# Kernel tuning notes

Measured on AMD Instinct MI355X. Metric: run time of the kernel, lower is better.

Reference implementation:

```python
import jax, jax.numpy as jnp
import numpy as np

N_NODES = 100_000
N_EDGES = 1_600_000
D_IN = 128
D_HID = 64   # hard-coded hidden width in Embedder.__init__
D_OUT = 128  # embed_dim
N_GRAPHS = 512


def setup_inputs() -> dict:
    key = jax.random.key(0)
    ks = jax.random.split(key, 10)
    x = jax.random.normal(ks[0], (N_NODES, D_IN), dtype=jnp.float32)
    edge_index = jax.random.randint(ks[1], (2, N_EDGES), 0, N_NODES, dtype=jnp.int64)
    batch_index = jnp.sort(jax.random.randint(ks[2], (N_NODES,), 0, N_GRAPHS, dtype=jnp.int64))
    def glorot(k, fan_in, fan_out):
        s = 1.0 / np.sqrt(fan_in)
        return jax.random.uniform(k, (fan_in, fan_out), jnp.float32, -s, s)
    # layer 1: SAGEConv(D_IN -> D_HID); layer 2: SAGEConv(D_HID -> D_OUT)
    return {
        "x": x,
        "W1_l": glorot(ks[3], D_IN, D_HID),   # applied to mean-aggregated neighbors
        "W1_r": glorot(ks[4], D_IN, D_HID),   # applied to root node
        "b1": jnp.zeros((D_HID,), jnp.float32),
        "W2_l": glorot(ks[5], D_HID, D_OUT),
        "W2_r": glorot(ks[6], D_HID, D_OUT),
        "b2": jnp.zeros((D_OUT,), jnp.float32),
        "edge_index": edge_index,
        "batch_index": batch_index,
    }


def _sage_conv(x, edge_index, W_l, W_r, b):
    # PyG SAGEConv with mean aggregation:
    # out_i = (mean_{j in N(i)} x_j) @ W_l + x_i @ W_r + b
    src, dst = edge_index[0], edge_index[1]
    n = x.shape[0]
    agg = jax.ops.segment_sum(x[src], dst, num_segments=n)          # [N, F]
    deg = jax.ops.segment_sum(jnp.ones((src.shape[0],), x.dtype), dst, num_segments=n)
    mean_nbr = agg / jnp.maximum(deg, 1.0)[:, None]
    return mean_nbr @ W_l + x @ W_r + b


def reference(x, W1_l, W1_r, b1, W2_l, W2_r, b2, edge_index, batch_index):
    h = _sage_conv(x, edge_index, W1_l, W1_r, b1)
    h = jax.nn.relu(h)
    h = _sage_conv(h, edge_index, W2_l, W2_r, b2)
    # F.dropout(p=0.5, training=False) -> identity in eval mode
    # gap: global mean pool per graph
    sums = jax.ops.segment_sum(h, batch_index, num_segments=N_GRAPHS)
    cnts = jax.ops.segment_sum(jnp.ones((h.shape[0],), h.dtype), batch_index, num_segments=N_GRAPHS)
    return sums / jnp.maximum(cnts, 1.0)[:, None]
```

## Files before the change

### kernel.cpp

```cpp
#include <hip/hip_runtime.h>

#define NN   100000
#define NE   1600000
#define DIN  128
#define DH   64
#define DOUT 128
#define NG   512

#define NB    391
#define PARTB 250
#define EPB   6400
#define CAP   5120

typedef short short8 __attribute__((ext_vector_type(8)));
typedef float floatx4 __attribute__((ext_vector_type(4)));

__device__ __forceinline__ unsigned short f2bf(float f) {
  unsigned b = __float_as_uint(f);
  b += 0x7FFF + ((b >> 16) & 1);
  return (unsigned short)(b >> 16);
}
__device__ __forceinline__ float bflo(unsigned u) {
  return __uint_as_float(u << 16);
}
__device__ __forceinline__ float bfhi(unsigned u) {
  return __uint_as_float(u & 0xFFFF0000u);
}
__device__ __forceinline__ unsigned pack2(float a, float b) {
  return (unsigned)f2bf(a) | ((unsigned)f2bf(b) << 16);
}

__global__ __launch_bounds__(256) void prep_kernel(
    int* __restrict__ gcur,
    const float* __restrict__ W1l, const float* __restrict__ W1r,
    short* __restrict__ wfrag, const int* __restrict__ batch,
    int* __restrict__ gs) {
  int b = blockIdx.x;
  if (b == 0) {
    for (int i = threadIdx.x; i < NB; i += 256) gcur[i] = i * CAP;
  } else if (b == 1) {
    for (int i = threadIdx.x; i < DIN * DH; i += 256) {
      int k = i >> 6, n = i & 63;
      int kt = k >> 5, kin = k & 31;
      int lane = ((kin >> 3) << 4) | (n & 15);
      int j8 = kin & 7;
      int jt = n >> 4;
      float wl = W1l[i], wr = W1r[i];
      unsigned bl_ = __float_as_uint(wl);
      unsigned br_ = __float_as_uint(wr);
      short hl = (short)(bl_ >> 16);
      short hr = (short)(br_ >> 16);
      float rl = wl - __uint_as_float(bl_ & 0xFFFF0000u);
      float rr = wr - __uint_as_float(br_ & 0xFFFF0000u);
      short ll = (short)(__float_as_uint(rl) >> 16);
      short lr = (short)(__float_as_uint(rr) >> 16);
      int base0 = (((kt * 2 + 0) * 4 + jt) * 2) * 512 + lane * 8 + j8;
      int base1 = (((kt * 2 + 1) * 4 + jt) * 2) * 512 + lane * 8 + j8;
      wfrag[base0]       = hl;
      wfrag[base0 + 512] = ll;
      wfrag[base1]       = hr;
      wfrag[base1 + 512] = lr;
    }
  } else {
    for (int g = threadIdx.x; g <= NG; g += 256) {
      if (g == NG) { gs[NG] = NN; continue; }
      int lo = 0, hi = NN;
      while (lo < hi) {
        int mid = (lo + hi) >> 1;
        if (batch[mid] < g) lo = mid + 1; else hi = mid;
      }
      gs[g] = lo;
    }
  }
}

__global__ __launch_bounds__(256, 4) void proj_part_kernel(
    const int* __restrict__ src, const int* __restrict__ dst,
    int* __restrict__ gcur, int* __restrict__ part,
    const float* __restrict__ x, const short* __restrict__ wfrag,
    const float* __restrict__ b1, unsigned short* __restrict__ xlb,
    unsigned short* __restrict__ xrb) {
  __shared__ short sB[16384];
  if (blockIdx.x < PARTB) {
    int* hist  = (int*)sB;
    int* base_ = hist + NB;
    int* lcur  = hist + 2 * NB;
    for (int i = threadIdx.x; i < NB; i += 256) hist[i] = 0;
    __syncthreads();
    int start = blockIdx.x * EPB;
    const int4* d4 = (const int4*)(dst + start);
    const int4* s4 = (const int4*)(src + start);
    for (int i = threadIdx.x; i < EPB / 4; i += 256) {
      int4 d = d4[i];
      atomicAdd(&hist[d.x >> 8], 1);
      atomicAdd(&hist[d.y >> 8], 1);
      atomicAdd(&hist[d.z >> 8], 1);
      atomicAdd(&hist[d.w >> 8], 1);
    }
    __syncthreads();
    for (int i = threadIdx.x; i < NB; i += 256) {
      base_[i] = atomicAdd(&gcur[i], hist[i]);
      lcur[i] = 0;
    }
    __syncthreads();
    for (int i = threadIdx.x; i < EPB / 4; i += 256) {
      int4 d = d4[i];
      int4 s = s4[i];
      int de[4] = {d.x, d.y, d.z, d.w};
      int se[4] = {s.x, s.y, s.z, s.w};
#pragma unroll
      for (int u = 0; u < 4; ++u) {
        int bkt = de[u] >> 8;
        int pos = base_[bkt] + atomicAdd(&lcur[bkt], 1);
        if (pos < (bkt + 1) * CAP)
          part[pos] = ((de[u] & 255) << 17) | se[u];
      }
    }
    return;
  }
  int wave = threadIdx.x >> 6;
  int lane = threadIdx.x & 63;
  int m = lane & 15, q = lane >> 4;
  int tpair = (blockIdx.x - PARTB) * 4 + wave;
  int tile0 = tpair * 2, tile1 = tile0 + 1;
  bool act0 = tile0 < 6250;
  bool act1 = tile1 < 6250;
  int t0c = act0 ? tile0 : 6249;
  int t1c = act1 ? tile1 : 6249;

  int r0 = t0c * 16 + m;
  int r1 = t1c * 16 + m;
  const float4* xa = (const float4*)x + (size_t)r0 * 32 + q * 2;
  const float4* xb = (const float4*)x + (size_t)r1 * 32 + q * 2;

  floatx4 acc0[8], acc1[8];
#pragma unroll
  for (int a = 0; a < 8; ++a) {
    acc0[a] = (floatx4){0.f, 0.f, 0.f, 0.f};
    acc1[a] = (floatx4){0.f, 0.f, 0.f, 0.f};
  }

  const float4* wf4 = (const float4*)wfrag;
  float4* sB4 = (float4*)sB;

#pragma unroll 1
  for (int stage = 0; stage < 2; ++stage) {
    if (stage) __syncthreads();
    for (int i = threadIdx.x; i < 2048; i += 256)
      sB4[i] = wf4[stage * 2048 + i];
    __syncthreads();

#pragma unroll
    for (int kk = 0; kk < 2; ++kk) {
      int kt = stage * 2 + kk;
      float4 p0 = xa[kt * 8];
      float4 p1 = xa[kt * 8 + 1];
      float4 p2 = xb[kt * 8];
      float4 p3 = xb[kt * 8 + 1];
      float af0[8] = {p0.x, p0.y, p0.z, p0.w, p1.x, p1.y, p1.z, p1.w};
      float af1[8] = {p2.x, p2.y, p2.z, p2.w, p3.x, p3.y, p3.z, p3.w};
      short8 ah0, al0, ah1, al1;
#pragma unroll
      for (int e = 0; e < 8; ++e) {
        unsigned b0 = __float_as_uint(af0[e]);
        ah0[e] = (short)(b0 >> 16);
        float lo0 = af0[e] - __uint_as_float(b0 & 0xFFFF0000u);
        al0[e] = (short)(__float_as_uint(lo0) >> 16);
        unsigned b1_ = __float_as_uint(af1[e]);
        ah1[e] = (short)(b1_ >> 16);
        float lo1 = af1[e] - __uint_as_float(b1_ & 0xFFFF0000u);
        al1[e] = (short)(__float_as_uint(lo1) >> 16);
      }
#pragma unroll
      for (int mat = 0; mat < 2; ++mat) {
#pragma unroll
        for (int jt = 0; jt < 4; ++jt) {
          int unit = ((kk * 2 + mat) * 4 + jt) * 2;
          short8 bh = *(const short8*)(sB + unit * 512 + lane * 8);
          short8 bl = *(const short8*)(sB + (unit + 1) * 512 + lane * 8);
          floatx4 c0 = acc0[mat * 4 + jt];
          c0 = __builtin_amdgcn_mfma_f32_16x16x32_bf16(ah0, bh, c0, 0, 0, 0);
          c0 = __builtin_amdgcn_mfma_f32_16x16x32_bf16(ah0, bl, c0, 0, 0, 0);
          c0 = __builtin_amdgcn_mfma_f32_16x16x32_bf16(al0, bh, c0, 0, 0, 0);
          acc0[mat * 4 + jt] = c0;
          floatx4 c1 = acc1[mat * 4 + jt];
          c1 = __builtin_amdgcn_mfma_f32_16x16x32_bf16(ah1, bh, c1, 0, 0, 0);
          c1 = __builtin_amdgcn_mfma_f32_16x16x32_bf16(ah1, bl, c1, 0, 0, 0);
          c1 = __builtin_amdgcn_mfma_f32_16x16x32_bf16(al1, bh, c1, 0, 0, 0);
          acc1[mat * 4 + jt] = c1;
        }
      }
    }
  }

#pragma unroll
  for (int jt = 0; jt < 4; ++jt) {
    int j = jt * 16 + m;
    float bj = b1[j];
    floatx4 cl0 = acc0[jt], cr0 = acc0[4 + jt];
    floatx4 cl1 = acc1[jt], cr1 = acc1[4 + jt];
    if (act0) {
#pragma unroll
      for (int r = 0; r < 4; ++r) {
        int n0 = tile0 * 16 + q * 4 + r;
        xlb[(size_t)n0 * DH + j] = f2bf(cl0[r]);
        xrb[(size_t)n0 * DH + j] = f2bf(cr0[r] + bj);
      }
    }
    if (act1) {
#pragma unroll
      for (int r = 0; r < 4; ++r) {
        int n1 = tile1 * 16 + q * 4 + r;
        xlb[(size_t)n1 * DH + j] = f2bf(cl1[r]);
        xrb[(size_t)n1 * DH + j] = f2bf(cr1[r] + bj);
      }
    }
  }
}

__global__ __launch_bounds__(256) void bucket_csr_kernel(
    const int* __restrict__ part, const int* __restrict__ gcur,
    int* __restrict__ row_start, int* __restrict__ row_end,
    int* __restrict__ eidx) {
  int b = blockIdx.x, t = threadIdx.x;
  int ebeg = b * CAP;
  int cnt_b = gcur[b] - ebeg; if (cnt_b > CAP) cnt_b = CAP;
  int eend = ebeg + cnt_b;
  int nvec = cnt_b >> 2;
  const int4* p4 = (const int4*)(part + ebeg);
  int nbase = b << 8;
  int nloc = NN - nbase; if (nloc > 256) nloc = 256;
  __shared__ int cntL[256];
  __shared__ int exclL[256];
  cntL[t] = 0;
  __syncthreads();
  for (int i = t; i < nvec; i += 256) {
    int4 v = p4[i];
    atomicAdd(&cntL[v.x >> 17], 1);
    atomicAdd(&cntL[v.y >> 17], 1);
    atomicAdd(&cntL[v.z >> 17], 1);
    atomicAdd(&cntL[v.w >> 17], 1);
  }
  for (int e = ebeg + (nvec << 2) + t; e < eend; e += 256)
    atomicAdd(&cntL[part[e] >> 17], 1);
  __syncthreads();
  int c = cntL[t];
  exclL[t] = c;
  __syncthreads();
  for (int off = 1; off < 256; off <<= 1) {
    int v = (t >= off) ? exclL[t - off] : 0;
    __syncthreads();
    exclL[t] += v;
    __syncthreads();
  }
  int excl = exclL[t] - c;
  if (t < nloc) {
    row_start[nbase + t] = ebeg + excl;
    row_end[nbase + t]   = ebeg + excl + c;
  }
  cntL[t] = excl;
  __syncthreads();
  for (int i = t; i < nvec; i += 256) {
    int4 v = p4[i];
    int ve[4] = {v.x, v.y, v.z, v.w};
#pragma unroll
    for (int u = 0; u < 4; ++u) {
      int pos = atomicAdd(&cntL[ve[u] >> 17], 1);
      eidx[ebeg + pos] = ve[u] & 0x1FFFF;
    }
  }
  for (int e = ebeg + (nvec << 2) + t; e < eend; e += 256) {
    int v = part[e];
    int pos = atomicAdd(&cntL[v >> 17], 1);
    eidx[ebeg + pos] = v & 0x1FFFF;
  }
}

template <bool RELU_ADD>
__global__ __launch_bounds__(256) void gather_kernel(
    const uint4* __restrict__ feat4, const int* __restrict__ row_start,
    const int* __restrict__ row_end, const int* __restrict__ eidx,
    const uint4* __restrict__ xr4, uint4* __restrict__ out4) {
  int t = blockIdx.x * 256 + threadIdx.x;
  int node = t >> 3;
  if (node >= NN) return;
  int fl = t & 7;
  int rs = row_start[node], re = row_end[node];
  float a0 = 0.f, a1 = 0.f, a2 = 0.f, a3 = 0.f;
  float a4 = 0.f, a5 = 0.f, a6 = 0.f, a7 = 0.f;
  int k = rs;
  for (; k + 8 <= re; k += 8) {
    uint4 v[8];
#pragma unroll
    for (int u = 0; u < 8; ++u) v[u] = feat4[(size_t)eidx[k + u] * 8 + fl];
#pragma unroll
    for (int u = 0; u < 8; ++u) {
      a0 += bflo(v[u].x); a1 += bfhi(v[u].x);
      a2 += bflo(v[u].y); a3 += bfhi(v[u].y);
      a4 += bflo(v[u].z); a5 += bfhi(v[u].z);
      a6 += bflo(v[u].w); a7 += bfhi(v[u].w);
    }
  }
  for (; k + 2 <= re; k += 2) {
    uint4 v0 = feat4[(size_t)eidx[k] * 8 + fl];
    uint4 v1 = feat4[(size_t)eidx[k + 1] * 8 + fl];
    a0 += bflo(v0.x) + bflo(v1.x); a1 += bfhi(v0.x) + bfhi(v1.x);
    a2 += bflo(v0.y) + bflo(v1.y); a3 += bfhi(v0.y) + bfhi(v1.y);
    a4 += bflo(v0.z) + bflo(v1.z); a5 += bfhi(v0.z) + bfhi(v1.z);
    a6 += bflo(v0.w) + bflo(v1.w); a7 += bfhi(v0.w) + bfhi(v1.w);
  }
  if (k < re) {
    uint4 v = feat4[(size_t)eidx[k] * 8 + fl];
    a0 += bflo(v.x); a1 += bfhi(v.x);
    a2 += bflo(v.y); a3 += bfhi(v.y);
    a4 += bflo(v.z); a5 += bfhi(v.z);
    a6 += bflo(v.w); a7 += bfhi(v.w);
  }
  float inv = 1.0f / fmaxf((float)(re - rs), 1.0f);
  a0 *= inv; a1 *= inv; a2 *= inv; a3 *= inv;
  a4 *= inv; a5 *= inv; a6 *= inv; a7 *= inv;
  if (RELU_ADD) {
    uint4 r = xr4[(size_t)node * 8 + fl];
    a0 = fmaxf(a0 + bflo(r.x), 0.f); a1 = fmaxf(a1 + bfhi(r.x), 0.f);
    a2 = fmaxf(a2 + bflo(r.y), 0.f); a3 = fmaxf(a3 + bfhi(r.y), 0.f);
    a4 = fmaxf(a4 + bflo(r.z), 0.f); a5 = fmaxf(a5 + bfhi(r.z), 0.f);
    a6 = fmaxf(a6 + bflo(r.w), 0.f); a7 = fmaxf(a7 + bfhi(r.w), 0.f);
  }
  uint4 o;
  o.x = pack2(a0, a1);
  o.y = pack2(a2, a3);
  o.z = pack2(a4, a5);
  o.w = pack2(a6, a7);
  out4[(size_t)node * 8 + fl] = o;
}

__global__ __launch_bounds__(1024) void gather2_pool_kernel(
    const uint4* __restrict__ feat4,
    const int* __restrict__ row_start, const int* __restrict__ row_end,
    const int* __restrict__ eidx,
    const int* __restrict__ gs, const float* __restrict__ W2l,
    const float* __restrict__ W2r, const float* __restrict__ b2,
    float* __restrict__ out) {
  int g = blockIdx.x;
  int start = gs[g], end = gs[g + 1];
  int slot = threadIdx.x >> 3;
  int fl   = threadIdx.x & 7;
  float sm[8], sh[8];
#pragma unroll
  for (int i = 0; i < 8; ++i) { sm[i] = 0.f; sh[i] = 0.f; }

  for (int n = start + slot; n < end; n += 128) {
    int rs = row_start[n], re = row_end[n];
    float a0 = 0.f, a1 = 0.f, a2 = 0.f, a3 = 0.f;
    float a4 = 0.f, a5 = 0.f, a6 = 0.f, a7 = 0.f;
    int k = rs;
    for (; k + 4 <= re; k += 4) {
      uint4 v[4];
#pragma unroll
      for (int u = 0; u < 4; ++u) v[u] = feat4[(size_t)eidx[k + u] * 8 + fl];
#pragma unroll
      for (int u = 0; u < 4; ++u) {
        a0 += bflo(v[u].x); a1 += bfhi(v[u].x);
        a2 += bflo(v[u].y); a3 += bfhi(v[u].y);
        a4 += bflo(v[u].z); a5 += bfhi(v[u].z);
        a6 += bflo(v[u].w); a7 += bfhi(v[u].w);
      }
    }
    for (; k < re; ++k) {
      uint4 v = feat4[(size_t)eidx[k] * 8 + fl];
      a0 += bflo(v.x); a1 += bfhi(v.x);
      a2 += bflo(v.y); a3 += bfhi(v.y);
      a4 += bflo(v.z); a5 += bfhi(v.z);
      a6 += bflo(v.w); a7 += bfhi(v.w);
    }
    float inv = 1.0f / fmaxf((float)(re - rs), 1.0f);
    sm[0] += a0 * inv; sm[1] += a1 * inv; sm[2] += a2 * inv; sm[3] += a3 * inv;
    sm[4] += a4 * inv; sm[5] += a5 * inv; sm[6] += a6 * inv; sm[7] += a7 * inv;
    uint4 hv = feat4[(size_t)n * 8 + fl];
    sh[0] += bflo(hv.x); sh[1] += bfhi(hv.x);
    sh[2] += bflo(hv.y); sh[3] += bfhi(hv.y);
    sh[4] += bflo(hv.z); sh[5] += bfhi(hv.z);
    sh[6] += bflo(hv.w); sh[7] += bfhi(hv.w);
  }

#pragma unroll
  for (int off = 8; off <= 32; off <<= 1) {
#pragma unroll
    for (int i = 0; i < 8; ++i) {
      sm[i] += __shfl_xor(sm[i], off);
      sh[i] += __shfl_xor(sh[i], off);
    }
  }

  __shared__ float redm[16][DH];
  __shared__ float redh[16][DH];
  int wv = threadIdx.x >> 6;
  int lane = threadIdx.x & 63;
  if (lane < 8) {
#pragma unroll
    for (int i = 0; i < 8; ++i) {
      redm[wv][lane * 8 + i] = sm[i];
      redh[wv][lane * 8 + i] = sh[i];
    }
  }
  __syncthreads();
  __shared__ float msL[DH], hsL[DH];
  if (threadIdx.x < DH) {
    float a = 0.f, b = 0.f;
#pragma unroll
    for (int w = 0; w < 16; ++w) { a += redm[w][threadIdx.x]; b += redh[w][threadIdx.x]; }
    msL[threadIdx.x] = a; hsL[threadIdx.x] = b;
  }
  __syncthreads();
  int j = threadIdx.x;
  if (j < DOUT) {
    float n_ = (float)(end - start);
    float acc = 0.f;
#pragma unroll 8
    for (int k = 0; k < DH; ++k)
      acc += msL[k] * W2l[k * DOUT + j] + hsL[k] * W2r[k * DOUT + j];
    out[g * DOUT + j] = (acc + n_ * b2[j]) / fmaxf(n_, 1.0f);
  }
}

extern "C" void kernel_launch(void* const* d_in, const int* in_sizes, int n_in,
                              void* d_out, int out_size, void* d_ws, size_t ws_size,
                              hipStream_t stream) {
  (void)in_sizes; (void)n_in; (void)out_size; (void)ws_size;
  const float* x   = (const float*)d_in[0];
  const float* W1l = (const float*)d_in[1];
  const float* W1r = (const float*)d_in[2];
  const float* b1  = (const float*)d_in[3];
  const float* W2l = (const float*)d_in[4];
  const float* W2r = (const float*)d_in[5];
  const float* b2  = (const float*)d_in[6];
  const int*   ei  = (const int*)d_in[7];
  const int*   batch = (const int*)d_in[8];
  const int* src = ei;
  const int* dst = ei + NE;
  float* out = (float*)d_out;

  char* ws = (char*)d_ws;
  unsigned short* xlb = (unsigned short*)(ws);
  unsigned short* hb  = (unsigned short*)(ws + 12800000);
  unsigned short* xrb = (unsigned short*)(ws + 38400000);
  int*  part      = (int*)(ws + 51200000);
  int*  gcur      = (int*)(ws + 59300000);
  int*  eidx      = (int*)(ws + 60000000);
  int*  row_start = (int*)(ws + 83200000);
  int*   gs       = (int*)(ws + 83600128);
  short* wfrag    = (short*)(ws + 83900032);
  int*  row_end   = (int*)(ws + 84000000);

  const int gBlocks = (NN * 8 + 255) / 256;

  prep_kernel<<<3, 256, 0, stream>>>(gcur, W1l, W1r, wfrag, batch, gs);

  proj_part_kernel<<<PARTB + 782, 256, 0, stream>>>(src, dst, gcur, part,
                                                    x, wfrag, b1, xlb, xrb);
  bucket_csr_kernel<<<NB, 256, 0, stream>>>(part, gcur, row_start, row_end, eidx);

  gather_kernel<true><<<gBlocks, 256, 0, stream>>>(
      (const uint4*)xlb, row_start, row_end, eidx, (const uint4*)xrb, (uint4*)hb);

  gather2_pool_kernel<<<NG, 1024, 0, stream>>>(
      (const uint4*)hb, row_start, row_end, eidx, gs, W2l, W2r, b2, out);
}
```

Before: 239.4 us.

## Fuse bucket CSR build with layer-1 gather using shared-memory edge lists

Merges the per-bucket CSR construction kernel and the first-layer mean-aggregation gather into one 1024-thread kernel per 256-node bucket. The sorted edge sources are kept in LDS and the row offsets in shared arrays, so the gather reads neighbor indices without a global round trip, and one kernel launch is removed. Global eidx and row arrays are still written for the second layer. The trade-off is only 391 blocks with about 22KB of LDS each, which limits the number of blocks in flight for the gather phase compared with the previous 3125-block launch.

```diff
diff --git a/kernel.cpp b/kernel.cpp
--- a/kernel.cpp
+++ b/kernel.cpp
@@ -218,120 +218,132 @@
   }
 }
 
-__global__ __launch_bounds__(256) void bucket_csr_kernel(
+__global__ __launch_bounds__(1024) void csr_gather1_kernel(
     const int* __restrict__ part, const int* __restrict__ gcur,
     int* __restrict__ row_start, int* __restrict__ row_end,
-    int* __restrict__ eidx) {
+    int* __restrict__ eidx,
+    const uint4* __restrict__ xlb4, const uint4* __restrict__ xrb4,
+    uint4* __restrict__ hb4) {
   int b = blockIdx.x, t = threadIdx.x;
   int ebeg = b * CAP;
   int cnt_b = gcur[b] - ebeg; if (cnt_b > CAP) cnt_b = CAP;
-  int eend = ebeg + cnt_b;
+  int nbase = b << 8;
+  int nloc = NN - nbase; if (nloc > 256) nloc = 256;
+
+  __shared__ int cntL[256];
+  __shared__ int lsA[256];
+  __shared__ int leA[256];
+  __shared__ int eidxL[CAP];
+
+  if (t < 256) cntL[t] = 0;
+  __syncthreads();
+
   int nvec = cnt_b >> 2;
   const int4* p4 = (const int4*)(part + ebeg);
-  int nbase = b << 8;
-  int nloc = NN - nbase; if (nloc > 256) nloc = 256;
-  __shared__ int cntL[256];
-  __shared__ int exclL[256];
-  cntL[t] = 0;
-  __syncthreads();
-  for (int i = t; i < nvec; i += 256) {
+  for (int i = t; i < nvec; i += 1024) {
     int4 v = p4[i];
     atomicAdd(&cntL[v.x >> 17], 1);
     atomicAdd(&cntL[v.y >> 17], 1);
     atomicAdd(&cntL[v.z >> 17], 1);
     atomicAdd(&cntL[v.w >> 17], 1);
   }
-  for (int e = ebeg + (nvec << 2) + t; e < eend; e += 256)
-    atomicAdd(&cntL[part[e] >> 17], 1);
-  __syncthreads();
-  int c = cntL[t];
-  exclL[t] = c;
+  for (int e = (nvec << 2) + t; e < cnt_b; e += 1024)
+    atomicAdd(&cntL[part[ebeg + e] >> 17], 1);
+  __syncthreads();
+
+  int c = 0;
+  if (t < 256) { c = cntL[t]; lsA[t] = c; }
   __syncthreads();
   for (int off = 1; off < 256; off <<= 1) {
-    int v = (t >= off) ? exclL[t - off] : 0;
-    __syncthreads();
-    exclL[t] += v;
-    __syncthreads();
-  }
-  int excl = exclL[t] - c;
-  if (t < nloc) {
-    row_start[nbase + t] = ebeg + excl;
-    row_end[nbase + t]   = ebeg + excl + c;
-  }
-  cntL[t] = excl;
-  __syncthreads();
-  for (int i = t; i < nvec; i += 256) {
+    int v = 0;
+    if (t < 256 && t >= off) v = lsA[t - off];
+    __syncthreads();
+    if (t < 256) lsA[t] += v;
+    __syncthreads();
+  }
+  if (t < 256) {
+    int excl = lsA[t] - c;
+    lsA[t] = excl;
+    leA[t] = excl + c;
+    if (t < nloc) {
+      row_start[nbase + t] = ebeg + excl;
+      row_end[nbase + t]   = ebeg + excl + c;
+    }
+    cntL[t] = excl;
+  }
+  __syncthreads();
+
+  for (int i = t; i < nvec; i += 1024) {
     int4 v = p4[i];
     int ve[4] = {v.x, v.y, v.z, v.w};
 #pragma unroll
     for (int u = 0; u < 4; ++u) {
       int pos = atomicAdd(&cntL[ve[u] >> 17], 1);
-      eidx[ebeg + pos] = ve[u] & 0x1FFFF;
-    }
-  }
-  for (int e = ebeg + (nvec << 2) + t; e < eend; e += 256) {
-    int v = part[e];
+      int s = ve[u] & 0x1FFFF;
+      eidxL[pos] = s;
+      eidx[ebeg + pos] = s;
+    }
+  }
+  for (int e = (nvec << 2) + t; e < cnt_b; e += 1024) {
+    int v = part[ebeg + e];
     int pos = atomicAdd(&cntL[v >> 17], 1);
-    eidx[ebeg + pos] = v & 0x1FFFF;
-  }
-}
-
-template <bool RELU_ADD>
-__global__ __launch_bounds__(256) void gather_kernel(
-    const uint4* __restrict__ feat4, const int* __restrict__ row_start,
-    const int* __restrict__ row_end, const int* __restrict__ eidx,
-    const uint4* __restrict__ xr4, uint4* __restrict__ out4) {
-  int t = blockIdx.x * 256 + threadIdx.x;
-  int node = t >> 3;
-  if (node >= NN) return;
+    int s = v & 0x1FFFF;
+    eidxL[pos] = s;
+    eidx[ebeg + pos] = s;
+  }
+  __syncthreads();
+
   int fl = t & 7;
-  int rs = row_start[node], re = row_end[node];
-  float a0 = 0.f, a1 = 0.f, a2 = 0.f, a3 = 0.f;
-  float a4 = 0.f, a5 = 0.f, a6 = 0.f, a7 = 0.f;
-  int k = rs;
-  for (; k + 8 <= re; k += 8) {
-    uint4 v[8];
-#pragma unroll
-    for (int u = 0; u < 8; ++u) v[u] = feat4[(size_t)eidx[k + u] * 8 + fl];
-#pragma unroll
-    for (int u = 0; u < 8; ++u) {
-      a0 += bflo(v[u].x); a1 += bfhi(v[u].x);
-      a2 += bflo(v[u].y); a3 += bfhi(v[u].y);
-      a4 += bflo(v[u].z); a5 += bfhi(v[u].z);
-      a6 += bflo(v[u].w); a7 += bfhi(v[u].w);
-    }
-  }
-  for (; k + 2 <= re; k += 2) {
-    uint4 v0 = feat4[(size_t)eidx[k] * 8 + fl];
-    uint4 v1 = feat4[(size_t)eidx[k + 1] * 8 + fl];
-    a0 += bflo(v0.x) + bflo(v1.x); a1 += bfhi(v0.x) + bfhi(v1.x);
-    a2 += bflo(v0.y) + bflo(v1.y); a3 += bfhi(v0.y) + bfhi(v1.y);
-    a4 += bflo(v0.z) + bflo(v1.z); a5 += bfhi(v0.z) + bfhi(v1.z);
-    a6 += bflo(v0.w) + bflo(v1.w); a7 += bfhi(v0.w) + bfhi(v1.w);
-  }
-  if (k < re) {
-    uint4 v = feat4[(size_t)eidx[k] * 8 + fl];
-    a0 += bflo(v.x); a1 += bfhi(v.x);
-    a2 += bflo(v.y); a3 += bfhi(v.y);
-    a4 += bflo(v.z); a5 += bfhi(v.z);
-    a6 += bflo(v.w); a7 += bfhi(v.w);
-  }
-  float inv = 1.0f / fmaxf((float)(re - rs), 1.0f);
-  a0 *= inv; a1 *= inv; a2 *= inv; a3 *= inv;
-  a4 *= inv; a5 *= inv; a6 *= inv; a7 *= inv;
-  if (RELU_ADD) {
-    uint4 r = xr4[(size_t)node * 8 + fl];
+  for (int pass = 0; pass < 2; ++pass) {
+    int nl = (t >> 3) + (pass << 7);
+    if (nl >= nloc) continue;
+    int rs = lsA[nl], re = leA[nl];
+    float a0 = 0.f, a1 = 0.f, a2 = 0.f, a3 = 0.f;
+    float a4 = 0.f, a5 = 0.f, a6 = 0.f, a7 = 0.f;
+    int k = rs;
+    for (; k + 8 <= re; k += 8) {
+      uint4 v[8];
+#pragma unroll
+      for (int u = 0; u < 8; ++u) v[u] = xlb4[(size_t)eidxL[k + u] * 8 + fl];
+#pragma unroll
+      for (int u = 0; u < 8; ++u) {
+        a0 += bflo(v[u].x); a1 += bfhi(v[u].x);
+        a2 += bflo(v[u].y); a3 += bfhi(v[u].y);
+        a4 += bflo(v[u].z); a5 += bfhi(v[u].z);
+        a6 += bflo(v[u].w); a7 += bfhi(v[u].w);
+      }
+    }
+    for (; k + 2 <= re; k += 2) {
+      uint4 v0 = xlb4[(size_t)eidxL[k] * 8 + fl];
+      uint4 v1 = xlb4[(size_t)eidxL[k + 1] * 8 + fl];
+      a0 += bflo(v0.x) + bflo(v1.x); a1 += bfhi(v0.x) + bfhi(v1.x);
+      a2 += bflo(v0.y) + bflo(v1.y); a3 += bfhi(v0.y) + bfhi(v1.y);
+      a4 += bflo(v0.z) + bflo(v1.z); a5 += bfhi(v0.z) + bfhi(v1.z);
+      a6 += bflo(v0.w) + bflo(v1.w); a7 += bfhi(v0.w) + bfhi(v1.w);
+    }
+    if (k < re) {
+      uint4 v = xlb4[(size_t)eidxL[k] * 8 + fl];
+      a0 += bflo(v.x); a1 += bfhi(v.x);
+      a2 += bflo(v.y); a3 += bfhi(v.y);
+      a4 += bflo(v.z); a5 += bfhi(v.z);
+      a6 += bflo(v.w); a7 += bfhi(v.w);
+    }
+    float inv = 1.0f / fmaxf((float)(re - rs), 1.0f);
+    a0 *= inv; a1 *= inv; a2 *= inv; a3 *= inv;
+    a4 *= inv; a5 *= inv; a6 *= inv; a7 *= inv;
+    int node = nbase + nl;
+    uint4 r = xrb4[(size_t)node * 8 + fl];
     a0 = fmaxf(a0 + bflo(r.x), 0.f); a1 = fmaxf(a1 + bfhi(r.x), 0.f);
     a2 = fmaxf(a2 + bflo(r.y), 0.f); a3 = fmaxf(a3 + bfhi(r.y), 0.f);
     a4 = fmaxf(a4 + bflo(r.z), 0.f); a5 = fmaxf(a5 + bfhi(r.z), 0.f);
     a6 = fmaxf(a6 + bflo(r.w), 0.f); a7 = fmaxf(a7 + bfhi(r.w), 0.f);
-  }
-  uint4 o;
-  o.x = pack2(a0, a1);
-  o.y = pack2(a2, a3);
-  o.z = pack2(a4, a5);
-  o.w = pack2(a6, a7);
-  out4[(size_t)node * 8 + fl] = o;
+    uint4 o;
+    o.x = pack2(a0, a1);
+    o.y = pack2(a2, a3);
+    o.z = pack2(a4, a5);
+    o.w = pack2(a6, a7);
+    hb4[(size_t)node * 8 + fl] = o;
+  }
 }
 
 __global__ __launch_bounds__(1024) void gather2_pool_kernel(
@@ -452,16 +464,14 @@
   short* wfrag    = (short*)(ws + 83900032);
   int*  row_end   = (int*)(ws + 84000000);
 
-  const int gBlocks = (NN * 8 + 255) / 256;
-
   prep_kernel<<<3, 256, 0, stream>>>(gcur, W1l, W1r, wfrag, batch, gs);
 
   proj_part_kernel<<<PARTB + 782, 256, 0, stream>>>(src, dst, gcur, part,
                                                     x, wfrag, b1, xlb, xrb);
-  bucket_csr_kernel<<<NB, 256, 0, stream>>>(part, gcur, row_start, row_end, eidx);
-
-  gather_kernel<true><<<gBlocks, 256, 0, stream>>>(
-      (const uint4*)xlb, row_start, row_end, eidx, (const uint4*)xrb, (uint4*)hb);
+
+  csr_gather1_kernel<<<NB, 1024, 0, stream>>>(
+      part, gcur, row_start, row_end, eidx,
+      (const uint4*)xlb, (const uint4*)xrb, (uint4*)hb);
 
   gather2_pool_kernel<<<NG, 1024, 0, stream>>>(
       (const uint4*)hb, row_start, row_end, eidx, gs, W2l, W2r, b2, out);
```

Measured after the change: 224.1 us. 1.07x faster.
